# Kernel tuning notes

Hardware: AMD Instinct MI355X
Metric: run time of the kernel (lower is better)

Reference implementation:

```python
import jax, jax.numpy as jnp
import numpy as np

# --- static hash-grid config (matches tcnn HashGrid in the torch module) ---
DIM = 3
N_LEVELS = 16
F = 2                      # n_features_per_level
LOG2_T = 19
T = 1 << LOG2_T            # hashmap size per level
BASE_RES = 16
TARGET_RES = 2048
PLS = float(np.exp2(np.log2(TARGET_RES / BASE_RES) / (N_LEVELS - 1)))  # per_level_scale
SCALES = [BASE_RES * PLS ** l for l in range(N_LEVELS)]
PRIMES = np.array([1, 2654435761, 805459861], dtype=np.uint32)
# 8 corner offsets of the unit cube, shape [8, 3]
OFFS = np.stack(np.meshgrid(*([np.arange(2)] * DIM), indexing='ij'), -1).reshape(-1, DIM).astype(np.float32)


def _hash(idx_u32):
    # idx_u32: [..., 3] uint32 -> [...] uint32 index into table of size T (power of 2)
    h = idx_u32[..., 0] * jnp.uint32(PRIMES[0])
    h = h ^ (idx_u32[..., 1] * jnp.uint32(PRIMES[1]))
    h = h ^ (idx_u32[..., 2] * jnp.uint32(PRIMES[2]))
    return h & jnp.uint32(T - 1)


def hashgrid_encode(x, table):
    # x: [N, 3] in [0,1); table: [L, T, F] fp32
    outs = []
    offs = jnp.asarray(OFFS)                      # [8, 3]
    for l in range(N_LEVELS):
        pos = x * jnp.float32(SCALES[l])          # [N, 3]
        base = jnp.floor(pos)
        frac = pos - base                         # [N, 3]
        corner = base[:, None, :] + offs[None]    # [N, 8, 3]
        idx = corner.astype(jnp.uint32)
        h = _hash(idx)                            # [N, 8]
        feat = table[l][h]                        # [N, 8, F] (gather)
        # trilinear weights: prod over dims of frac or (1-frac)
        w = jnp.prod(jnp.where(offs[None] > 0.5, frac[:, None, :], 1.0 - frac[:, None, :]), axis=-1)  # [N, 8]
        outs.append(jnp.sum(w[..., None] * feat, axis=1))  # [N, F]
    return jnp.concatenate(outs, axis=-1)         # [N, L*F] = [N, 32]


def setup_inputs() -> dict:
    key = jax.random.key(0)
    ks = jax.random.split(key, 8)
    N = 1048576
    dim_in = N_LEVELS * F          # 32
    hid = 16                       # (16+15)//16*16
    dout = 16                      # grid_output_dim
    x = jax.random.uniform(ks[0], (N, DIM), dtype=jnp.float32)
    table = jax.random.uniform(ks[1], (N_LEVELS, T, F), dtype=jnp.float32, minval=-1e-4, maxval=1e-4)
    def lin(k, fi, fo):
        b = 1.0 / np.sqrt(fi)
        return jax.random.uniform(k, (fo, fi), dtype=jnp.float32, minval=-b, maxval=b)
    W0 = lin(ks[2], dim_in, hid); b0 = jnp.zeros((hid,), jnp.float32)
    W1 = lin(ks[3], hid, hid);    b1 = jnp.zeros((hid,), jnp.float32)
    W2 = lin(ks[4], hid, dout);   b2 = jnp.zeros((dout,), jnp.float32)
    return {"x": x, "table": table, "W0": W0, "b0": b0, "W1": W1, "b1": b1, "W2": W2, "b2": b2}


def reference(x, table, W0, b0, W1, b1, W2, b2):
    h = hashgrid_encode(x, table)                 # [N, 32]
    h = jax.nn.relu(h @ W0.T + b0)
    h = jax.nn.relu(h @ W1.T + b1)
    return h @ W2.T + b2                          # [N, 16]
```

## Files before the change

### kernel.cpp

```cpp
#include <hip/hip_runtime.h>
#include <math.h>

#define NLV 16
#define LOG2_T 19
#define T_SIZE (1u << LOG2_T)
#define T_MASK (T_SIZE - 1u)
#define P2 2654435761u
#define P3 805459861u
#define NBUCK 32768

typedef float vf2 __attribute__((ext_vector_type(2)));
typedef float vf4 __attribute__((ext_vector_type(4)));

struct Scales { float s[NLV]; };

__device__ __forceinline__ unsigned mpart(unsigned v) {
    v = (v | (v << 8)) & 0x100Fu;
    v = (v | (v << 4)) & 0x10C3u;
    v = (v | (v << 2)) & 0x1249u;
    return v;
}
__device__ __forceinline__ unsigned mkey(float px, float py, float pz) {
    unsigned cx = (unsigned)(px * 32.f); cx = cx > 31u ? 31u : cx;
    unsigned cy = (unsigned)(py * 32.f); cy = cy > 31u ? 31u : cy;
    unsigned cz = (unsigned)(pz * 32.f); cz = cz > 31u ? 31u : cz;
    return mpart(cx) | (mpart(cy) << 1) | (mpart(cz) << 2);
}

__global__ __launch_bounds__(256) void zero_hist_kernel(unsigned* hist) {
    int i = blockIdx.x * 256 + threadIdx.x;
    if (i < NBUCK) hist[i] = 0u;
}

__global__ __launch_bounds__(256) void hist_kernel(
    const float* __restrict__ x, unsigned* __restrict__ hist, int N)
{
    const int i = blockIdx.x * 256 + threadIdx.x;
    if (i >= N) return;
    const float px = x[3 * (size_t)i + 0];
    const float py = x[3 * (size_t)i + 1];
    const float pz = x[3 * (size_t)i + 2];
    atomicAdd(&hist[mkey(px, py, pz)], 1u);
}

__global__ __launch_bounds__(1024) void scan_kernel(unsigned* hist) {
    __shared__ unsigned tot[1024];
    const int t = threadIdx.x;
    const unsigned base = (unsigned)t * 32u;
    unsigned loc[32];
    unsigned s = 0;
    #pragma unroll
    for (int k = 0; k < 32; ++k) { loc[k] = s; s += hist[base + k]; }
    tot[t] = s;
    __syncthreads();
    for (int off = 1; off < 1024; off <<= 1) {
        unsigned u = (t >= off) ? tot[t - off] : 0u;
        __syncthreads();
        tot[t] += u;
        __syncthreads();
    }
    const unsigned excl = tot[t] - s;
    #pragma unroll
    for (int k = 0; k < 32; ++k) hist[base + k] = excl + loc[k];
}

__global__ __launch_bounds__(256) void scatter_kernel(
    const float* __restrict__ x, unsigned* __restrict__ cursor,
    vf4* __restrict__ xs, int N)
{
    const int i = blockIdx.x * 256 + threadIdx.x;
    if (i >= N) return;
    const float px = x[3 * (size_t)i + 0];
    const float py = x[3 * (size_t)i + 1];
    const float pz = x[3 * (size_t)i + 2];
    const unsigned key = mkey(px, py, pz);
    const unsigned pos = atomicAdd(&cursor[key], 1u);
    vf4 v; v[0] = px; v[1] = py; v[2] = pz; v[3] = __int_as_float(i);
    xs[pos] = v;
}

__device__ __forceinline__ void enc_level(
    float px, float py, float pz, float s, const float* __restrict__ tl,
    float& f0, float& f1)
{
    const float fx = px * s, fy = py * s, fz = pz * s;
    const float bx = floorf(fx), by = floorf(fy), bz = floorf(fz);
    const float rx = fx - bx, ry = fy - by, rz = fz - bz;
    const unsigned ix0 = (unsigned)bx, iy0 = (unsigned)by, iz0 = (unsigned)bz;
    const unsigned hy0 = iy0 * P2, hy1 = (iy0 + 1u) * P2;
    const unsigned hz0 = iz0 * P3, hz1 = (iz0 + 1u) * P3;
    const float wx0 = 1.f - rx, wy0 = 1.f - ry, wz0 = 1.f - rz;
    f0 = 0.f; f1 = 0.f;
    if (!(ix0 & 1u)) {
        float c0[8], c1[8];
        #pragma unroll
        for (int yz = 0; yz < 4; ++yz) {
            const unsigned r = ((yz & 2) ? hy1 : hy0) ^ ((yz & 1) ? hz1 : hz0);
            const unsigned h0 = (ix0 ^ r) & T_MASK;
            const vf4 q = *(const vf4*)(tl + 2u * (size_t)(h0 & ~1u));
            const bool odd = (h0 & 1u) != 0u;
            c0[yz]     = odd ? q[2] : q[0];
            c1[yz]     = odd ? q[3] : q[1];
            c0[4 + yz] = odd ? q[0] : q[2];
            c1[4 + yz] = odd ? q[1] : q[3];
        }
        #pragma unroll
        for (int c = 0; c < 8; ++c) {
            const float w = ((c & 4) ? rx : wx0) * ((c & 2) ? ry : wy0) * ((c & 1) ? rz : wz0);
            f0 += w * c0[(c >> 2) * 4 + (c & 3)];
            f1 += w * c1[(c >> 2) * 4 + (c & 3)];
        }
    } else {
        const unsigned hx0 = ix0, hx1 = ix0 + 1u;
        #pragma unroll
        for (int c = 0; c < 8; ++c) {
            unsigned h = ((c & 4) ? hx1 : hx0) ^ ((c & 2) ? hy1 : hy0) ^ ((c & 1) ? hz1 : hz0);
            h &= T_MASK;
            const vf2 f = *(const vf2*)(tl + 2u * (size_t)h);
            const float w = ((c & 4) ? rx : wx0) * ((c & 2) ? ry : wy0) * ((c & 1) ? rz : wz0);
            f0 += w * f[0];
            f1 += w * f[1];
        }
    }
}

__global__ __launch_bounds__(256) void encode_coarse_kernel(
    const vf4* __restrict__ xs, const float* __restrict__ table,
    float* __restrict__ enc, int N, Scales sc)
{
    int i = blockIdx.x * 256 + threadIdx.x;
    if (i >= N) return;
    const vf4 p = xs[i];
    #pragma unroll
    for (int l = 0; l < 5; ++l) {
        float f0, f1;
        enc_level(p[0], p[1], p[2], sc.s[l], table + (size_t)l * T_SIZE * 2u, f0, f1);
        vf2 v; v[0] = f0; v[1] = f1;
        *(vf2*)(enc + ((size_t)l * N + i) * 2u) = v;
    }
}

template<int LVL>
__global__ __launch_bounds__(256) void encode_fine_kernel(
    const vf4* __restrict__ xs, const float* __restrict__ tl, float s,
    float* __restrict__ encl, int N)
{
    const int i0 = blockIdx.x * 1024 + threadIdx.x;
    #pragma unroll
    for (int k = 0; k < 4; ++k) {
        const int i = i0 + k * 256;
        if (i < N) {
            const vf4 p = xs[i];
            float f0, f1;
            enc_level(p[0], p[1], p[2], s, tl, f0, f1);
            vf2 v; v[0] = f0; v[1] = f1;
            *(vf2*)(encl + (size_t)i * 2u) = v;
        }
    }
}

__global__ __launch_bounds__(256) void mlp_kernel(
    const float* __restrict__ enc, const vf4* __restrict__ xs,
    const float* __restrict__ W0, const float* __restrict__ b0,
    const float* __restrict__ W1, const float* __restrict__ b1,
    const float* __restrict__ W2, const float* __restrict__ b2,
    float* __restrict__ out, int N)
{
    __shared__ float st[256 * 17];
    const int base = blockIdx.x * 512;
    const int t = threadIdx.x;
    const float* xsf = (const float*)xs;

    #pragma unroll
    for (int q = 0; q < 2; ++q) {
        if (q) __syncthreads();
        const int i = base + q * 256 + t;
        if (i < N) {
            vf2 e2[16];
            #pragma unroll
            for (int l = 0; l < NLV; ++l)
                e2[l] = *(const vf2*)(enc + ((size_t)l * N + i) * 2u);

            vf2 a0v[8];
            #pragma unroll
            for (int j = 0; j < 16; ++j) {
                vf2 acc = {0.f, 0.f};
                #pragma unroll
                for (int l = 0; l < 16; ++l)
                    acc += e2[l] * *(const vf2*)(W0 + j * 32 + 2 * l);
                a0v[j >> 1][j & 1] = fmaxf(b0[j] + acc[0] + acc[1], 0.f);
            }
            vf2 a1v[8];
            #pragma unroll
            for (int j = 0; j < 16; ++j) {
                vf2 acc = {0.f, 0.f};
                #pragma unroll
                for (int k = 0; k < 8; ++k)
                    acc += a0v[k] * *(const vf2*)(W1 + j * 16 + 2 * k);
                a1v[j >> 1][j & 1] = fmaxf(b1[j] + acc[0] + acc[1], 0.f);
            }
            #pragma unroll
            for (int j = 0; j < 16; ++j) {
                vf2 acc = {0.f, 0.f};
                #pragma unroll
                for (int k = 0; k < 8; ++k)
                    acc += a1v[k] * *(const vf2*)(W2 + j * 16 + 2 * k);
                st[t * 17 + j] = b2[j] + acc[0] + acc[1];
            }
        }
        __syncthreads();

        const int c = t & 3;
        #pragma unroll
        for (int w = 0; w < 4; ++w) {
            const int p = (t >> 2) + w * 64;
            const int gi = base + q * 256 + p;
            if (gi < N) {
                const int dst = __float_as_int(xsf[4 * (size_t)gi + 3]);
                const vf4 v = *(const vf4*)&st[p * 17 + 4 * c];
                __builtin_nontemporal_store(v, (vf4*)(out + 16 * (size_t)dst + 4 * c));
            }
        }
    }
}

__global__ __launch_bounds__(256) void encode_coarse_unsorted_kernel(
    const float* __restrict__ x, const float* __restrict__ table,
    float* __restrict__ enc, int N, Scales sc)
{
    int i = blockIdx.x * 256 + threadIdx.x;
    if (i >= N) return;
    const float px = x[3 * (size_t)i + 0];
    const float py = x[3 * (size_t)i + 1];
    const float pz = x[3 * (size_t)i + 2];
    #pragma unroll
    for (int l = 0; l < 5; ++l) {
        float f0, f1;
        enc_level(px, py, pz, sc.s[l], table + (size_t)l * T_SIZE * 2u, f0, f1);
        vf2 v; v[0] = f0; v[1] = f1;
        *(vf2*)(enc + ((size_t)l * N + i) * 2u) = v;
    }
}
__global__ __launch_bounds__(256) void encode_one_unsorted_kernel(
    const float* __restrict__ x, const float* __restrict__ tl, float s,
    float* __restrict__ encl, int N)
{
    int i = blockIdx.x * 256 + threadIdx.x;
    if (i >= N) return;
    const float px = x[3 * (size_t)i + 0];
    const float py = x[3 * (size_t)i + 1];
    const float pz = x[3 * (size_t)i + 2];
    float f0, f1;
    enc_level(px, py, pz, s, tl, f0, f1);
    vf2 v; v[0] = f0; v[1] = f1;
    *(vf2*)(encl + (size_t)i * 2u) = v;
}
__global__ __launch_bounds__(256) void mlp_noperm_kernel(
    const float* __restrict__ enc,
    const float* __restrict__ W0, const float* __restrict__ b0,
    const float* __restrict__ W1, const float* __restrict__ b1,
    const float* __restrict__ W2, const float* __restrict__ b2,
    float* __restrict__ out, int N)
{
    int i = blockIdx.x * 256 + threadIdx.x;
    if (i >= N) return;
    float e[32];
    #pragma unroll
    for (int l = 0; l < NLV; ++l) {
        vf2 v = *(const vf2*)(enc + ((size_t)l * N + i) * 2u);
        e[2 * l + 0] = v[0];
        e[2 * l + 1] = v[1];
    }
    float a0[16];
    #pragma unroll
    for (int j = 0; j < 16; ++j) {
        float s = b0[j];
        #pragma unroll
        for (int k = 0; k < 32; ++k) s += e[k] * W0[j * 32 + k];
        a0[j] = fmaxf(s, 0.f);
    }
    float a1[16];
    #pragma unroll
    for (int j = 0; j < 16; ++j) {
        float s = b1[j];
        #pragma unroll
        for (int k = 0; k < 16; ++k) s += a0[k] * W1[j * 16 + k];
        a1[j] = fmaxf(s, 0.f);
    }
    #pragma unroll
    for (int j = 0; j < 16; ++j) {
        float s = b2[j];
        #pragma unroll
        for (int k = 0; k < 16; ++k) s += a1[k] * W2[j * 16 + k];
        out[16 * (size_t)i + j] = s;
    }
}
__global__ __launch_bounds__(256) void tcnn_fused_kernel(
    const float* __restrict__ x, const float* __restrict__ table,
    const float* __restrict__ W0, const float* __restrict__ b0,
    const float* __restrict__ W1, const float* __restrict__ b1,
    const float* __restrict__ W2, const float* __restrict__ b2,
    float* __restrict__ out, int N, Scales sc)
{
    int i = blockIdx.x * blockDim.x + threadIdx.x;
    if (i >= N) return;
    const float px = x[3 * (size_t)i + 0];
    const float py = x[3 * (size_t)i + 1];
    const float pz = x[3 * (size_t)i + 2];
    float e[32];
    #pragma unroll
    for (int l = 0; l < NLV; ++l) {
        float f0, f1;
        enc_level(px, py, pz, sc.s[l], table + (size_t)l * T_SIZE * 2u, f0, f1);
        e[2 * l] = f0; e[2 * l + 1] = f1;
    }
    float a0[16];
    #pragma unroll
    for (int j = 0; j < 16; ++j) {
        float s = b0[j];
        #pragma unroll
        for (int k = 0; k < 32; ++k) s += e[k] * W0[j * 32 + k];
        a0[j] = fmaxf(s, 0.f);
    }
    float a1[16];
    #pragma unroll
    for (int j = 0; j < 16; ++j) {
        float s = b1[j];
        #pragma unroll
        for (int k = 0; k < 16; ++k) s += a0[k] * W1[j * 16 + k];
        a1[j] = fmaxf(s, 0.f);
    }
    #pragma unroll
    for (int j = 0; j < 16; ++j) {
        float s = b2[j];
        #pragma unroll
        for (int k = 0; k < 16; ++k) s += a1[k] * W2[j * 16 + k];
        out[16 * (size_t)i + j] = s;
    }
}

extern "C" void kernel_launch(void* const* d_in, const int* in_sizes, int n_in,
                              void* d_out, int out_size, void* d_ws, size_t ws_size,
                              hipStream_t stream) {
    const float* x     = (const float*)d_in[0];
    const float* table = (const float*)d_in[1];
    const float* W0    = (const float*)d_in[2];
    const float* b0    = (const float*)d_in[3];
    const float* W1    = (const float*)d_in[4];
    const float* b1    = (const float*)d_in[5];
    const float* W2    = (const float*)d_in[6];
    const float* b2    = (const float*)d_in[7];
    float* out = (float*)d_out;

    const int N = in_sizes[0] / 3;

    Scales sc;
    const double pls = exp2(log2(2048.0 / 16.0) / 15.0);
    for (int l = 0; l < NLV; ++l) sc.s[l] = (float)(16.0 * pow(pls, (double)l));

    const int block = 256;
    const int grid = (N + block - 1) / block;

    const size_t encB  = (size_t)N * 2u * NLV * sizeof(float);
    const size_t xsB   = (size_t)N * sizeof(float) * 4u;
    const size_t histB = (size_t)NBUCK * sizeof(unsigned);

    if (ws_size >= encB + xsB + histB) {
        float*    enc  = (float*)d_ws;
        vf4*      xs   = (vf4*)((char*)d_ws + encB);
        unsigned* hist = (unsigned*)((char*)d_ws + encB + xsB);

        zero_hist_kernel<<<(NBUCK + 255) / 256, block, 0, stream>>>(hist);
        hist_kernel<<<grid, block, 0, stream>>>(x, hist, N);
        scan_kernel<<<1, 1024, 0, stream>>>(hist);
        scatter_kernel<<<grid, block, 0, stream>>>(x, hist, xs, N);

        encode_coarse_kernel<<<grid, block, 0, stream>>>(xs, table, enc, N, sc);

        const int gridQ = (N + 1023) / 1024;
        #define LAUNCH_FINE(L) \
            encode_fine_kernel<L><<<gridQ, block, 0, stream>>>( \
                xs, table + (size_t)(L) * T_SIZE * 2u, sc.s[(L)], \
                enc + (size_t)(L) * (size_t)N * 2u, N)
        LAUNCH_FINE(5);  LAUNCH_FINE(6);  LAUNCH_FINE(7);  LAUNCH_FINE(8);
        LAUNCH_FINE(9);  LAUNCH_FINE(10); LAUNCH_FINE(11); LAUNCH_FINE(12);
        LAUNCH_FINE(13); LAUNCH_FINE(14); LAUNCH_FINE(15);
        #undef LAUNCH_FINE

        const int gridM = (N + 511) / 512;
        mlp_kernel<<<gridM, block, 0, stream>>>(enc, xs, W0, b0, W1, b1, W2, b2, out, N);
    } else if (ws_size >= encB) {
        float* enc = (float*)d_ws;
        encode_coarse_unsorted_kernel<<<grid, block, 0, stream>>>(x, table, enc, N, sc);
        for (int l = 5; l < NLV; ++l) {
            encode_one_unsorted_kernel<<<grid, block, 0, stream>>>(
                x, table + (size_t)l * T_SIZE * 2u, sc.s[l],
                enc + (size_t)l * (size_t)N * 2u, N);
        }
        mlp_noperm_kernel<<<grid, block, 0, stream>>>(enc, W0, b0, W1, b1, W2, b2, out, N);
    } else {
        tcnn_fused_kernel<<<grid, block, 0, stream>>>(x, table, W0, b0, W1, b1, W2, b2,
                                                      out, N, sc);
    }
}
```

Baseline: 504.2 us.

## Repack coarse hash-grid levels into dense linear grids before encoding

Adds a repack kernel that, on every call, materialises levels 0-7 of the hash table as dense D^3 grids, where D is roughly the level resolution plus two, rounded up to even. Encoding for those levels then indexes neighbouring corners linearly instead of through the hash. The aim is to replace scattered hashed gathers with spatially coherent loads on the sorted points, giving better cache-line reuse. The dense grids live in the workspace slot of encoder levels 9-15, which is only written later. The cost is an extra pass that writes about D^3 cells per level, growing quickly at level 7, plus an additional launch.

```diff
diff --git a/kernel.cpp b/kernel.cpp
--- a/kernel.cpp
+++ b/kernel.cpp
@@ -13,6 +13,11 @@
 typedef float vf4 __attribute__((ext_vector_type(4)));
 
 struct Scales { float s[NLV]; };
+struct RpCfg {
+    unsigned cellOff[9];
+    unsigned D[8];
+    unsigned long long rpOff[8];
+};
 
 __device__ __forceinline__ unsigned mpart(unsigned v) {
     v = (v | (v << 8)) & 0x100Fu;
@@ -77,6 +82,82 @@
     const unsigned pos = atomicAdd(&cursor[key], 1u);
     vf4 v; v[0] = px; v[1] = py; v[2] = pz; v[3] = __int_as_float(i);
     xs[pos] = v;
+}
+
+__global__ __launch_bounds__(256) void repack_all_kernel(
+    const float* __restrict__ table, float* __restrict__ rp, RpCfg cfg)
+{
+    const unsigned tid = blockIdx.x * 256 + threadIdx.x;
+    if (tid >= cfg.cellOff[8]) return;
+    unsigned l = 0;
+    #pragma unroll
+    for (int k = 1; k < 8; ++k) if (tid >= cfg.cellOff[k]) l = k;
+    const unsigned c = tid - cfg.cellOff[l];
+    const unsigned D = cfg.D[l];
+    const unsigned ix = c % D;
+    const unsigned t2 = c / D;
+    const unsigned iy = t2 % D;
+    const unsigned iz = t2 / D;
+    const unsigned h = (ix ^ (iy * P2) ^ (iz * P3)) & T_MASK;
+    const float* tl = table + (size_t)l * T_SIZE * 2u;
+    *(vf2*)(rp + cfg.rpOff[l] + 2u * (size_t)c) = *(const vf2*)(tl + 2u * (size_t)h);
+}
+
+__device__ __forceinline__ void enc_level_lin(
+    float px, float py, float pz, float s, const float* __restrict__ rp, unsigned D,
+    float& f0, float& f1)
+{
+    const float fx = px * s, fy = py * s, fz = pz * s;
+    const float bx = floorf(fx), by = floorf(fy), bz = floorf(fz);
+    const float rx = fx - bx, ry = fy - by, rz = fz - bz;
+    const unsigned ix0 = (unsigned)bx, iy0 = (unsigned)by, iz0 = (unsigned)bz;
+    const float wx0 = 1.f - rx, wy0 = 1.f - ry, wz0 = 1.f - rz;
+    const unsigned D2 = D * D;
+    const unsigned base = (iz0 * D + iy0) * D + ix0;
+    f0 = 0.f; f1 = 0.f;
+    #pragma unroll
+    for (int c = 0; c < 8; ++c) {
+        const unsigned idx = base + ((c & 4) ? 1u : 0u) + ((c & 2) ? D : 0u) + ((c & 1) ? D2 : 0u);
+        const vf2 f = *(const vf2*)(rp + 2u * (size_t)idx);
+        const float w = ((c & 4) ? rx : wx0) * ((c & 2) ? ry : wy0) * ((c & 1) ? rz : wz0);
+        f0 += w * f[0];
+        f1 += w * f[1];
+    }
+}
+
+__global__ __launch_bounds__(256) void encode_coarse_lin_kernel(
+    const vf4* __restrict__ xs, const float* __restrict__ rp,
+    float* __restrict__ enc, int N, Scales sc, RpCfg cfg)
+{
+    int i = blockIdx.x * 256 + threadIdx.x;
+    if (i >= N) return;
+    const vf4 p = xs[i];
+    #pragma unroll
+    for (int l = 0; l < 5; ++l) {
+        float f0, f1;
+        enc_level_lin(p[0], p[1], p[2], sc.s[l], rp + cfg.rpOff[l], cfg.D[l], f0, f1);
+        vf2 v; v[0] = f0; v[1] = f1;
+        *(vf2*)(enc + ((size_t)l * N + i) * 2u) = v;
+    }
+}
+
+template<int LVL>
+__global__ __launch_bounds__(256) void encode_fine_lin_kernel(
+    const vf4* __restrict__ xs, const float* __restrict__ rpl, unsigned D, float s,
+    float* __restrict__ encl, int N)
+{
+    const int i0 = blockIdx.x * 1024 + threadIdx.x;
+    #pragma unroll
+    for (int k = 0; k < 4; ++k) {
+        const int i = i0 + k * 256;
+        if (i < N) {
+            const vf4 p = xs[i];
+            float f0, f1;
+            enc_level_lin(p[0], p[1], p[2], s, rpl, D, f0, f1);
+            vf2 v; v[0] = f0; v[1] = f1;
+            *(vf2*)(encl + (size_t)i * 2u) = v;
+        }
+    }
 }
 
 __device__ __forceinline__ void enc_level(
@@ -358,12 +439,32 @@
     const double pls = exp2(log2(2048.0 / 16.0) / 15.0);
     for (int l = 0; l < NLV; ++l) sc.s[l] = (float)(16.0 * pow(pls, (double)l));
 
+    RpCfg cfg;
+    {
+        unsigned long long off = 0;
+        unsigned cells = 0;
+        for (int l = 0; l < 8; ++l) {
+            int D = (int)floor((double)sc.s[l]) + 2;
+            if (D & 1) ++D;
+            cfg.D[l] = (unsigned)D;
+            cfg.cellOff[l] = cells;
+            cfg.rpOff[l] = off;
+            const unsigned c = (unsigned)D * (unsigned)D * (unsigned)D;
+            cells += c;
+            off += 2ull * c;
+        }
+        cfg.cellOff[8] = cells;
+    }
+    const unsigned long long rpFloats = cfg.rpOff[7] +
+        2ull * cfg.D[7] * cfg.D[7] * cfg.D[7];
+
     const int block = 256;
     const int grid = (N + block - 1) / block;
 
     const size_t encB  = (size_t)N * 2u * NLV * sizeof(float);
     const size_t xsB   = (size_t)N * sizeof(float) * 4u;
     const size_t histB = (size_t)NBUCK * sizeof(unsigned);
+    const bool rpFits = rpFloats <= (unsigned long long)(NLV - 9) * (size_t)N * 2u;
 
     if (ws_size >= encB + xsB + histB) {
         float*    enc  = (float*)d_ws;
@@ -375,16 +476,37 @@
         scan_kernel<<<1, 1024, 0, stream>>>(hist);
         scatter_kernel<<<grid, block, 0, stream>>>(x, hist, xs, N);
 
-        encode_coarse_kernel<<<grid, block, 0, stream>>>(xs, table, enc, N, sc);
-
         const int gridQ = (N + 1023) / 1024;
+
+        if (rpFits) {
+            float* rp = enc + (size_t)9 * N * 2u;
+            const int gridR = (int)((cfg.cellOff[8] + 255u) / 256u);
+            repack_all_kernel<<<gridR, block, 0, stream>>>(table, rp, cfg);
+
+            encode_coarse_lin_kernel<<<grid, block, 0, stream>>>(xs, rp, enc, N, sc, cfg);
+
+            #define LAUNCH_FINE_LIN(L) \
+                encode_fine_lin_kernel<L><<<gridQ, block, 0, stream>>>( \
+                    xs, rp + cfg.rpOff[(L)], cfg.D[(L)], sc.s[(L)], \
+                    enc + (size_t)(L) * (size_t)N * 2u, N)
+            LAUNCH_FINE_LIN(5); LAUNCH_FINE_LIN(6); LAUNCH_FINE_LIN(7);
+            #undef LAUNCH_FINE_LIN
+        } else {
+            encode_coarse_kernel<<<grid, block, 0, stream>>>(xs, table, enc, N, sc);
+            #define LAUNCH_FINE_H(L) \
+                encode_fine_kernel<L><<<gridQ, block, 0, stream>>>( \
+                    xs, table + (size_t)(L) * T_SIZE * 2u, sc.s[(L)], \
+                    enc + (size_t)(L) * (size_t)N * 2u, N)
+            LAUNCH_FINE_H(5); LAUNCH_FINE_H(6); LAUNCH_FINE_H(7);
+            #undef LAUNCH_FINE_H
+        }
+
         #define LAUNCH_FINE(L) \
             encode_fine_kernel<L><<<gridQ, block, 0, stream>>>( \
                 xs, table + (size_t)(L) * T_SIZE * 2u, sc.s[(L)], \
                 enc + (size_t)(L) * (size_t)N * 2u, N)
-        LAUNCH_FINE(5);  LAUNCH_FINE(6);  LAUNCH_FINE(7);  LAUNCH_FINE(8);
-        LAUNCH_FINE(9);  LAUNCH_FINE(10); LAUNCH_FINE(11); LAUNCH_FINE(12);
-        LAUNCH_FINE(13); LAUNCH_FINE(14); LAUNCH_FINE(15);
+        LAUNCH_FINE(8);  LAUNCH_FINE(9);  LAUNCH_FINE(10); LAUNCH_FINE(11);
+        LAUNCH_FINE(12); LAUNCH_FINE(13); LAUNCH_FINE(14); LAUNCH_FINE(15);
         #undef LAUNCH_FINE
 
         const int gridM = (N + 511) / 512;
```

After: 516.1 us. +2.3%, slower.
